# Kernel tuning notes

Hardware: AMD Instinct MI355X
Metric: run time of the kernel (lower is better)

## Reference

```python
import jax, jax.numpy as jnp
import numpy as np

B, T, N = 8, 168, 1024
FD, FS, FF = 16, 32, 8
DL, DG, HE, E = 128, 128, 4, 16384
BN = B * N


def _lstm_last(x, Wih, Whh, bih, bhh):
    # x: (BN, T, FD); PyTorch gate order i, f, g, o
    h0 = jnp.zeros((x.shape[0], Whh.shape[1]), x.dtype)
    def step(carry, xt):
        h, c = carry
        g = xt @ Wih.T + h @ Whh.T + bih + bhh
        i, f, gg, o = jnp.split(g, 4, axis=-1)
        c = jax.nn.sigmoid(f) * c + jax.nn.sigmoid(i) * jnp.tanh(gg)
        h = jax.nn.sigmoid(o) * jnp.tanh(c)
        return (h, c), None
    (h, _), _ = jax.lax.scan(step, (h0, h0), jnp.swapaxes(x, 0, 1))
    return h


def _ln(x, g, b):
    mu = x.mean(-1, keepdims=True)
    v = ((x - mu) ** 2).mean(-1, keepdims=True)
    return (x - mu) / jnp.sqrt(v + 1e-5) * g + b


def _gat(x, src, dst, ea, W, a_src, a_dst, a_edge, We, bias):
    # PyG GATConv: concat=False (mean over heads), edge_dim=1, LeakyReLU(0.2)
    xl = (x @ W.T).reshape(BN, HE, -1)                 # (BN, H, C)
    as_ = jnp.sum(xl * a_src, -1)                      # (BN, H)
    ad_ = jnp.sum(xl * a_dst, -1)
    ep = (ea @ We.T).reshape(-1, HE, xl.shape[-1])     # (Eb, H, C)
    ae_ = jnp.sum(ep * a_edge, -1)                     # (Eb, H)
    alpha = jax.nn.leaky_relu(as_[src] + ad_[dst] + ae_, 0.2)
    amax = jax.ops.segment_max(alpha, dst, num_segments=BN)
    ex = jnp.exp(alpha - amax[dst])
    den = jax.ops.segment_sum(ex, dst, num_segments=BN)
    w = ex / den[dst]                                  # softmax over incoming edges
    out = jax.ops.segment_sum(w[:, :, None] * xl[src], dst, num_segments=BN)
    return out.mean(axis=1) + bias


def _forward(fl, edge_index):
    (dyn, fcst, sta, ew,
     lWih, lWhh, lbih, lbhh, sW, sb, fW, fb, uW, ub,
     g0W, g0as, g0ad, g0ae, g0We, g0b,
     g1W, g1as, g1ad, g1ae, g1We, g1b,
     n0g, n0b, n1g, n1b, oW, ob) = fl
    x = jnp.transpose(dyn, (0, 2, 1, 3)).reshape(BN, T, FD)
    z = _lstm_last(x, lWih, lWhh, lbih, lbhh)
    s = jax.nn.relu(sta.reshape(BN, -1) @ sW.T + sb)
    f = jax.nn.relu(fcst.reshape(BN, -1) @ fW.T + fb)
    h = jax.nn.relu(jnp.concatenate([z, s, f], -1) @ uW.T + ub)
    # batch the graph: B disjoint copies with node offsets
    off = (jnp.arange(B) * N)[:, None]
    src = (edge_index[0][None] + off).reshape(-1)
    dst = (edge_index[1][None] + off).reshape(-1)
    ea = jnp.tile(ew.reshape(-1, 1), (B, 1))           # (B*E, 1)
    # PyG GATConv default add_self_loops=True, fill_value='mean' of incoming edge attrs
    deg = jax.ops.segment_sum(jnp.ones_like(ea), dst, num_segments=BN)
    loop_ea = jax.ops.segment_sum(ea, dst, num_segments=BN) / jnp.maximum(deg, 1.0)
    loops = jnp.arange(BN)
    src = jnp.concatenate([src, loops])
    dst = jnp.concatenate([dst, loops])
    ea = jnp.concatenate([ea, loop_ea], 0)
    # hop 0: relu on delta (not last hop), residual (res_proj=None since DL==DG), LayerNorm
    d0 = jax.nn.relu(_gat(h, src, dst, ea, g0W, g0as, g0ad, g0ae, g0We, g0b))
    h = _ln(h + d0, n0g, n0b)
    # hop 1: last hop, no relu on delta
    d1 = _gat(h, src, dst, ea, g1W, g1as, g1ad, g1ae, g1We, g1b)
    h = _ln(h + d1, n1g, n1b)
    return (h @ oW.T + ob).reshape(B, N)


def setup_inputs():
    key = jax.random.key(0)
    ks = iter(jax.random.split(key, 48))
    def rn(shape, s=0.08):
        return jax.random.normal(next(ks), shape, jnp.float32) * s
    HO = HE * DG  # heads * out_channels
    return dict(
        dynamic_features=rn((B, T, N, FD), 1.0),
        forecast_features=rn((B, N, FF), 1.0),
        static_features=rn((B, N, FS), 1.0),
        edge_index=jax.random.randint(next(ks), (2, E), 0, N),
        edge_weight=jax.random.uniform(next(ks), (E,), jnp.float32),
        lstm_Wih=rn((4 * DL, FD)), lstm_Whh=rn((4 * DL, DL)),
        lstm_bih=rn((4 * DL,)), lstm_bhh=rn((4 * DL,)),
        static_W=rn((DL, FS)), static_b=rn((DL,)),
        fcst_W=rn((DL, FF)), fcst_b=rn((DL,)),
        fusion_W=rn((DL, 3 * DL)), fusion_b=rn((DL,)),
        gat0_W=rn((HO, DL)), gat0_att_src=rn((1, HE, DG)), gat0_att_dst=rn((1, HE, DG)),
        gat0_att_edge=rn((1, HE, DG)), gat0_We=rn((HO, 1)), gat0_bias=rn((DG,)),
        gat1_W=rn((HO, DG)), gat1_att_src=rn((1, HE, DG)), gat1_att_dst=rn((1, HE, DG)),
        gat1_att_edge=rn((1, HE, DG)), gat1_We=rn((HO, 1)), gat1_bias=rn((DG,)),
        ln0_g=jnp.ones((DG,), jnp.float32), ln0_b=jnp.zeros((DG,), jnp.float32),
        ln1_g=jnp.ones((DG,), jnp.float32), ln1_b=jnp.zeros((DG,), jnp.float32),
        out_W=rn((1, DG)), out_b=rn((1,)),
    )


def reference(dynamic_features, forecast_features, static_features, edge_weight,
              lstm_Wih, lstm_Whh, lstm_bih, lstm_bhh, static_W, static_b,
              fcst_W, fcst_b, fusion_W, fusion_b,
              gat0_W, gat0_att_src, gat0_att_dst, gat0_att_edge, gat0_We, gat0_bias,
              gat1_W, gat1_att_src, gat1_att_dst, gat1_att_edge, gat1_We, gat1_bias,
              ln0_g, ln0_b, ln1_g, ln1_b, out_W, out_b, edge_index):
    fl = (dynamic_features, forecast_features, static_features, edge_weight,
          lstm_Wih, lstm_Whh, lstm_bih, lstm_bhh, static_W, static_b,
          fcst_W, fcst_b, fusion_W, fusion_b,
          gat0_W, gat0_att_src, gat0_att_dst, gat0_att_edge, gat0_We, gat0_bias,
          gat1_W, gat1_att_src, gat1_att_dst, gat1_att_edge, gat1_We, gat1_bias,
          ln0_g, ln0_b, ln1_g, ln1_b, out_W, out_b)
    return _forward(fl, edge_index)
```

## Files before the change

### kernel.cpp

```cpp
#include <hip/hip_runtime.h>
#include <hip/hip_bf16.h>
#include <stdint.h>

#define BB 8
#define TT 168
#define NN 1024
#define BN_ 8192
#define FD_ 16
#define EE 16384

typedef short short8 __attribute__((ext_vector_type(8)));
typedef __bf16 bf16x8 __attribute__((ext_vector_type(8)));
typedef float f32x4 __attribute__((ext_vector_type(4)));

#if __has_builtin(__builtin_amdgcn_exp2f)
#define EXP2(x) __builtin_amdgcn_exp2f(x)
#else
#define EXP2(x) exp2f(x)
#endif
#if __has_builtin(__builtin_amdgcn_rcpf)
#define RCPF(x) __builtin_amdgcn_rcpf(x)
#else
#define RCPF(x) (1.f / (x))
#endif
#define L2E 1.4426950408889634f
#define T2E 2.8853900817779268f

static __device__ __forceinline__ float b2f(ushort s) {
    unsigned u = ((unsigned)s) << 16;
    return __builtin_bit_cast(float, u);
}
static __device__ __forceinline__ ushort f2b(float f) {
    unsigned u = __builtin_bit_cast(unsigned, f);
    unsigned lsb = (u >> 16) & 1u;
    u += 0x7fffu + lsb;
    return (ushort)(u >> 16);
}
static __device__ __forceinline__ ushort f2b_fast(float f) {
    unsigned u = __builtin_bit_cast(unsigned, f);
    return (ushort)((u + 0x8000u) >> 16);
}
static __device__ __forceinline__ f32x4 mfma16(short8 a, short8 b, f32x4 c) {
    return __builtin_amdgcn_mfma_f32_16x16x32_bf16(
        __builtin_bit_cast(bf16x8, a), __builtin_bit_cast(bf16x8, b), c, 0, 0, 0);
}

#define O_WIH 0
#define O_WHH 8192
#define O_STA 73728
#define O_FCS 335872
#define O_SW  401408
#define O_FW  405504
#define O_UW  406528
#define O_G0W 455680
#define O_G1W 521216
#define O_END 586752

__global__ void cast_kernel(const float* __restrict__ Wih, const float* __restrict__ Whh,
                            const float* __restrict__ sta, const float* __restrict__ fcst,
                            const float* __restrict__ sW, const float* __restrict__ fW,
                            const float* __restrict__ uW, const float* __restrict__ g0W,
                            const float* __restrict__ g1W, ushort* __restrict__ dst) {
    const int i = blockIdx.x * 256 + threadIdx.x;
    if (i >= O_END) return;
    float v;
    if      (i < O_WHH) v = Wih[i - O_WIH];
    else if (i < O_STA) v = Whh[i - O_WHH];
    else if (i < O_FCS) v = sta[i - O_STA];
    else if (i < O_SW)  v = fcst[i - O_FCS];
    else if (i < O_FW)  v = sW[i - O_SW];
    else if (i < O_UW)  v = fW[i - O_FW];
    else if (i < O_G0W) v = uW[i - O_UW];
    else if (i < O_G1W) v = g0W[i - O_G0W];
    else                v = g1W[i - O_G1W];
    dst[i] = f2b(v);
}

__global__ __launch_bounds__(1024) void prep_kernel(
    const int* __restrict__ ei, const float* __restrict__ ew,
    const float* __restrict__ We0, const float* __restrict__ ae0,
    const float* __restrict__ We1, const float* __restrict__ ae1,
    int* __restrict__ deg0, int* __restrict__ offs, float* __restrict__ loopea,
    int* __restrict__ eidx, float* __restrict__ se) {
    __shared__ int degL[1024];
    __shared__ float wsL[1024];
    __shared__ int sc[1024];
    __shared__ float seL[8];
    const int t = threadIdx.x;
    degL[t] = 0; wsL[t] = 0.f;
    if (t < 8) seL[t] = 0.f;
    __syncthreads();
    for (int e = t; e < EE; e += 1024) {
        const int d = ei[EE + e];
        atomicAdd(&degL[d], 1);
        atomicAdd(&wsL[d], ew[e]);
    }
    __syncthreads();
    const int d = degL[t];
    sc[t] = d;
    __syncthreads();
    for (int o = 1; o < 1024; o <<= 1) {
        const int v = (t >= o) ? sc[t - o] : 0;
        __syncthreads();
        sc[t] += v;
        __syncthreads();
    }
    const int excl = sc[t] - d;
    offs[t] = excl;
    deg0[t] = d;
    loopea[t] = wsL[t] / fmaxf((float)d, 1.f);
    degL[t] = excl;
    __syncthreads();
    for (int e = t; e < EE; e += 1024) {
        const int dd = ei[EE + e];
        const int slot = atomicAdd(&degL[dd], 1);
        eidx[slot] = e;
    }
    const int g = t >> 7, k = t & 127;
    const int head = g & 3;
    const float* W = (g >> 2) ? We1 : We0;
    const float* A = (g >> 2) ? ae1 : ae0;
    atomicAdd(&seL[g], W[head * 128 + k] * A[head * 128 + k]);
    __syncthreads();
    if (t < 8) se[t] = seL[t];
}

__global__ __launch_bounds__(256, 2) void lstm_kernel(
    const float* __restrict__ dyn,
    const ushort* __restrict__ Wih,
    const ushort* __restrict__ Whh,
    const float* __restrict__ bih,
    const float* __restrict__ bhh,
    ushort* __restrict__ zsf)
{
    constexpr int HS = 168;
    __shared__ ushort hbuf[2][16 * HS];

    const int tid = threadIdx.x;
    const int blk = blockIdx.x;
    const int b = blk >> 6;
    const int n0 = (blk & 63) << 4;
    const int w = tid >> 6, lane = tid & 63, quad = lane >> 4, m = lane & 15;

    short8 Bf[5][4][2];
    float ci[2], cf[2], cg[2], co[2];
#pragma unroll
    for (int jj = 0; jj < 2; jj++) {
        const int u = (2 * w + jj) * 16 + m;
#pragma unroll
        for (int g = 0; g < 4; g++) {
            const int grow = g * 128 + u;
#pragma unroll
            for (int kt = 0; kt < 4; kt++)
                Bf[kt][g][jj] = *(const short8*)(Whh + grow * 128 + kt * 32 + quad * 8);
            if (quad < 2) Bf[4][g][jj] = *(const short8*)(Wih + grow * 16 + quad * 8);
            else          Bf[4][g][jj] = short8{0, 0, 0, 0, 0, 0, 0, 0};
        }
        ci[jj] = -L2E * (bih[u] + bhh[u]);
        cf[jj] = -L2E * (bih[128 + u] + bhh[128 + u]);
        cg[jj] =  T2E * (bih[256 + u] + bhh[256 + u]);
        co[jj] = -L2E * (bih[384 + u] + bhh[384 + u]);
    }

    float c[2][4];
#pragma unroll
    for (int jj = 0; jj < 2; jj++)
#pragma unroll
        for (int r = 0; r < 4; r++) c[jj][r] = 0.f;

    for (int i = tid; i < 2 * 16 * HS; i += 256) ((ushort*)hbuf)[i] = 0;
    __syncthreads();

    const int xn = tid >> 4, xf = tid & 15;
    const size_t xbase = (size_t)b * TT * NN * FD_ + (size_t)(n0 + xn) * FD_ + xf;
    hbuf[0][xn * HS + 128 + xf] = f2b(dyn[xbase]);
    float xv = dyn[xbase + (size_t)NN * FD_];
    __syncthreads();

    for (int t = 0; t < TT; t++) {
        const ushort* rb = hbuf[t & 1];
        ushort* wb = hbuf[(t + 1) & 1];
        if (t + 1 < TT) wb[xn * HS + 128 + xf] = f2b(xv);
        if (t + 2 < TT) xv = dyn[xbase + (size_t)(t + 2) * NN * FD_];

        f32x4 acc[4][2];
#pragma unroll
        for (int g = 0; g < 4; g++)
#pragma unroll
            for (int jj = 0; jj < 2; jj++) acc[g][jj] = f32x4{0.f, 0.f, 0.f, 0.f};
#pragma unroll
        for (int kt = 0; kt < 5; kt++) {
            short8 a = *(const short8*)&rb[m * HS + kt * 32 + quad * 8];
#pragma unroll
            for (int g = 0; g < 4; g++)
#pragma unroll
                for (int jj = 0; jj < 2; jj++)
                    acc[g][jj] = mfma16(a, Bf[kt][g][jj], acc[g][jj]);
        }

#pragma unroll
        for (int jj = 0; jj < 2; jj++) {
            const int u = (2 * w + jj) * 16 + m;
#pragma unroll
            for (int r = 0; r < 4; r++) {
                const int n = quad * 4 + r;
                const float Di = 1.f + EXP2(fmaf(acc[0][jj][r], -L2E, ci[jj]));
                const float Df = 1.f + EXP2(fmaf(acc[1][jj][r], -L2E, cf[jj]));
                const float Eg = EXP2(fmaf(acc[2][jj][r], T2E, cg[jj]));
                const float Do = 1.f + EXP2(fmaf(acc[3][jj][r], -L2E, co[jj]));
                const float R  = RCPF(Di * (1.f + Eg));
                const float sf = RCPF(Df);
                const float cc = fmaf(sf, c[jj][r], (Eg - 1.f) * R);
                c[jj][r] = cc;
                const float Ec = EXP2(T2E * cc);
                const float h = (Ec - 1.f) * RCPF(Do * (1.f + Ec));
                wb[n * HS + u] = f2b_fast(h);
                if (t == TT - 1) zsf[(size_t)(blk * 16 + n) * 384 + u] = f2b_fast(h);
            }
        }
        __syncthreads();
    }
}

__global__ __launch_bounds__(256) void gemm_sf_kernel(
    const ushort* __restrict__ staB, const ushort* __restrict__ sWB,
    const float* __restrict__ sb,
    const ushort* __restrict__ fcsB, const ushort* __restrict__ fWB,
    const float* __restrict__ fb, ushort* __restrict__ zsf) {
    const int tid = threadIdx.x;
    const int lane = tid & 63, quad = lane >> 4, m = lane & 15;
    int wave = blockIdx.x * 4 + (tid >> 6);
    const short8 z8 = short8{0, 0, 0, 0, 0, 0, 0, 0};
    short8 a, bf;
    int r0, c0, ocol;
    const float* bias;
    if (wave < 4096) {
        r0 = (wave >> 3) * 16; c0 = (wave & 7) * 16; ocol = 128; bias = sb;
        a  = *(const short8*)(staB + (size_t)(r0 + m) * 32 + quad * 8);
        bf = *(const short8*)(sWB + (size_t)(c0 + m) * 32 + quad * 8);
    } else {
        wave -= 4096;
        r0 = (wave >> 3) * 16; c0 = (wave & 7) * 16; ocol = 256; bias = fb;
        a  = (quad == 0) ? *(const short8*)(fcsB + (size_t)(r0 + m) * 8) : z8;
        bf = (quad == 0) ? *(const short8*)(fWB + (size_t)(c0 + m) * 8) : z8;
    }
    f32x4 acc = mfma16(a, bf, f32x4{0.f, 0.f, 0.f, 0.f});
    const float bv = bias[c0 + m];
#pragma unroll
    for (int r = 0; r < 4; r++) {
        const int row = r0 + quad * 4 + r;
        zsf[(size_t)row * 384 + ocol + c0 + m] = f2b(fmaxf(acc[r] + bv, 0.f));
    }
}

__global__ __launch_bounds__(256) void gemm_fusion_kernel(
    const ushort* __restrict__ A, const ushort* __restrict__ Bt,
    const float* __restrict__ bias, ushort* __restrict__ hB, float* __restrict__ hF) {
    const int tid = threadIdx.x;
    const int lane = tid & 63, quad = lane >> 4, m = lane & 15;
    const int wave = blockIdx.x * 4 + (tid >> 6);
    const int r0 = (wave >> 3) * 16, c0 = (wave & 7) * 16;
    f32x4 acc = f32x4{0.f, 0.f, 0.f, 0.f};
#pragma unroll
    for (int kt = 0; kt < 12; kt++) {
        const int k = kt * 32 + quad * 8;
        short8 a  = *(const short8*)(A + (size_t)(r0 + m) * 384 + k);
        short8 bf = *(const short8*)(Bt + (size_t)(c0 + m) * 384 + k);
        acc = mfma16(a, bf, acc);
    }
    const int col = c0 + m;
    const float bv = bias[col];
#pragma unroll
    for (int r = 0; r < 4; r++) {
        const int row = r0 + quad * 4 + r;
        const float v = fmaxf(acc[r] + bv, 0.f);
        hB[(size_t)row * 128 + col] = f2b(v);
        hF[(size_t)row * 128 + col] = v;
    }
}

__global__ __launch_bounds__(256) void gemmatt_kernel(
    const ushort* __restrict__ hB, const ushort* __restrict__ W,
    const float* __restrict__ asrc, const float* __restrict__ adst,
    ushort* __restrict__ xl, float* __restrict__ as_, float* __restrict__ ad_) {
    const int tid = threadIdx.x;
    const int lane = tid & 63, quad = lane >> 4, m = lane & 15;
    const int w = tid >> 6;
    const int r0 = blockIdx.x * 16;
    f32x4 acc[8];
#pragma unroll
    for (int ct = 0; ct < 8; ct++) acc[ct] = f32x4{0.f, 0.f, 0.f, 0.f};
#pragma unroll
    for (int kt = 0; kt < 4; kt++) {
        const int k = kt * 32 + quad * 8;
        short8 a = *(const short8*)(hB + (size_t)(r0 + m) * 128 + k);
#pragma unroll
        for (int ct = 0; ct < 8; ct++) {
            short8 bf = *(const short8*)(W + (size_t)(w * 128 + ct * 16 + m) * 128 + k);
            acc[ct] = mfma16(a, bf, acc[ct]);
        }
    }
    float sa[4] = {0.f, 0.f, 0.f, 0.f}, sd[4] = {0.f, 0.f, 0.f, 0.f};
#pragma unroll
    for (int ct = 0; ct < 8; ct++) {
        const int col = w * 128 + ct * 16 + m;
        const float av = asrc[col], dv = adst[col];
#pragma unroll
        for (int r = 0; r < 4; r++) {
            const float v = acc[ct][r];
            xl[(size_t)(r0 + quad * 4 + r) * 512 + col] = f2b(v);
            sa[r] = fmaf(v, av, sa[r]);
            sd[r] = fmaf(v, dv, sd[r]);
        }
    }
#pragma unroll
    for (int o = 1; o < 16; o <<= 1) {
#pragma unroll
        for (int r = 0; r < 4; r++) {
            sa[r] += __shfl_xor(sa[r], o);
            sd[r] += __shfl_xor(sd[r], o);
        }
    }
    if (m == 0) {
#pragma unroll
        for (int r = 0; r < 4; r++) {
            const int node = r0 + quad * 4 + r;
            as_[node * 4 + w] = sa[r];
            ad_[node * 4 + w] = sd[r];
        }
    }
}

__global__ __launch_bounds__(256) void edge_exp_kernel(
    const int* __restrict__ ei, const float* __restrict__ ew,
    const float* __restrict__ as_, const float* __restrict__ ad_,
    const float* __restrict__ se4, float* __restrict__ pexp) {
    const int idx = blockIdx.x * 256 + threadIdx.x;
    const int b = idx >> 14, e = idx & (EE - 1);
    const int src = b * 1024 + ei[e];
    const int dst = b * 1024 + ei[EE + e];
    const float eaw = ew[e];
    const float4 s4 = *(const float4*)(as_ + src * 4);
    const float4 d4 = *(const float4*)(ad_ + dst * 4);
    float4 p;
    float* pp = (float*)&p;
    const float* s = (const float*)&s4;
    const float* d = (const float*)&d4;
#pragma unroll
    for (int h = 0; h < 4; h++) {
        float a = s[h] + d[h] + eaw * se4[h];
        a = (a < 0.f) ? 0.2f * a : a;
        pp[h] = EXP2(fminf(a, 60.f) * L2E);
    }
    *(float4*)(pexp + (size_t)idx * 4) = p;
}

__global__ __launch_bounds__(256) void gat_kernel(
    float* __restrict__ hF, ushort* __restrict__ hB, const ushort* __restrict__ xl,
    const float* __restrict__ as_, const float* __restrict__ ad_,
    const float* __restrict__ pexp,
    const int* __restrict__ eidx, const int* __restrict__ offs,
    const int* __restrict__ deg0, const float* __restrict__ loopea,
    const int* __restrict__ ei,
    const float* __restrict__ se4, const float* __restrict__ bias,
    const float* __restrict__ lng, const float* __restrict__ lnb, int relu,
    int writeOut, const float* __restrict__ oW, const float* __restrict__ ob,
    float* __restrict__ out) {
    const int lane = threadIdx.x & 63;
    const int v = blockIdx.x * 4 + (threadIdx.x >> 6);
    const int b = v >> 10, n = v & 1023;
    const int dg = deg0[n], off = offs[n];

    const float lea = loopea[n];
    const float4 s4 = *(const float4*)(as_ + v * 4);
    const float4 d4 = *(const float4*)(ad_ + v * 4);
    const float* sp = (const float*)&s4;
    const float* dp = (const float*)&d4;
    float den[4], num0[4], num1[4];
#pragma unroll
    for (int h = 0; h < 4; h++) {
        float a = sp[h] + dp[h] + lea * se4[h];
        a = (a < 0.f) ? 0.2f * a : a;
        const float p = EXP2(fminf(a, 60.f) * L2E);
        den[h] = p;
        num0[h] = p * b2f(xl[(size_t)v * 512 + h * 128 + lane]);
        num1[h] = p * b2f(xl[(size_t)v * 512 + h * 128 + 64 + lane]);
    }
    for (int i = 0; i < dg; i++) {
        const int e = eidx[off + i];
        const int src = b * 1024 + ei[e];
        const float4 p4 = *(const float4*)(pexp + (size_t)(b * EE + e) * 4);
        const float* p = (const float*)&p4;
        const ushort* xr = xl + (size_t)src * 512;
#pragma unroll
        for (int h = 0; h < 4; h++) {
            den[h] += p[h];
            num0[h] = fmaf(p[h], b2f(xr[h * 128 + lane]), num0[h]);
            num1[h] = fmaf(p[h], b2f(xr[h * 128 + 64 + lane]), num1[h]);
        }
    }
    float o0 = 0.f, o1 = 0.f;
#pragma unroll
    for (int h = 0; h < 4; h++) {
        const float inv = RCPF(den[h]);
        o0 = fmaf(num0[h], inv, o0);
        o1 = fmaf(num1[h], inv, o1);
    }

    float d0 = o0 * 0.25f + bias[lane];
    float d1 = o1 * 0.25f + bias[64 + lane];
    if (relu) { d0 = fmaxf(d0, 0.f); d1 = fmaxf(d1, 0.f); }
    const float x0 = hF[(size_t)v * 128 + lane] + d0;
    const float x1 = hF[(size_t)v * 128 + 64 + lane] + d1;

    float s = x0 + x1;
#pragma unroll
    for (int o = 32; o; o >>= 1) s += __shfl_xor(s, o);
    const float mu = s * (1.f / 128.f);
    const float e0 = x0 - mu, e1 = x1 - mu;
    float vs = e0 * e0 + e1 * e1;
#pragma unroll
    for (int o = 32; o; o >>= 1) vs += __shfl_xor(vs, o);
    const float r = rsqrtf(vs * (1.f / 128.f) + 1e-5f);
    const float y0 = e0 * r * lng[lane] + lnb[lane];
    const float y1 = e1 * r * lng[64 + lane] + lnb[64 + lane];
    if (writeOut) {
        float t = y0 * oW[lane] + y1 * oW[64 + lane];
#pragma unroll
        for (int o = 32; o; o >>= 1) t += __shfl_xor(t, o);
        if (lane == 0) out[v] = t + ob[0];
    } else {
        hF[(size_t)v * 128 + lane] = y0;
        hF[(size_t)v * 128 + 64 + lane] = y1;
        hB[(size_t)v * 128 + lane] = f2b(y0);
        hB[(size_t)v * 128 + 64 + lane] = f2b(y1);
    }
}

extern "C" void kernel_launch(void* const* d_in, const int* in_sizes, int n_in,
                              void* d_out, int out_size, void* d_ws, size_t ws_size,
                              hipStream_t stream) {
    const float* dyn  = (const float*)d_in[0];
    const float* fcst = (const float*)d_in[1];
    const float* sta  = (const float*)d_in[2];
    const int*   ei   = (const int*)d_in[3];
    const float* ew   = (const float*)d_in[4];
    const float* lWih = (const float*)d_in[5];
    const float* lWhh = (const float*)d_in[6];
    const float* lbih = (const float*)d_in[7];
    const float* lbhh = (const float*)d_in[8];
    const float* sW = (const float*)d_in[9];
    const float* sb = (const float*)d_in[10];
    const float* fW = (const float*)d_in[11];
    const float* fb = (const float*)d_in[12];
    const float* uW = (const float*)d_in[13];
    const float* ub = (const float*)d_in[14];
    const float* g0W  = (const float*)d_in[15];
    const float* g0as = (const float*)d_in[16];
    const float* g0ad = (const float*)d_in[17];
    const float* g0ae = (const float*)d_in[18];
    const float* g0We = (const float*)d_in[19];
    const float* g0b  = (const float*)d_in[20];
    const float* g1W  = (const float*)d_in[21];
    const float* g1as = (const float*)d_in[22];
    const float* g1ad = (const float*)d_in[23];
    const float* g1ae = (const float*)d_in[24];
    const float* g1We = (const float*)d_in[25];
    const float* g1b  = (const float*)d_in[26];
    const float* ln0g = (const float*)d_in[27];
    const float* ln0b = (const float*)d_in[28];
    const float* ln1g = (const float*)d_in[29];
    const float* ln1b = (const float*)d_in[30];
    const float* oW = (const float*)d_in[31];
    const float* ob = (const float*)d_in[32];

    char* p = (char*)d_ws;
    ushort* castB = (ushort*)p; p += (size_t)O_END * 2 + 512;
    ushort* zsf = (ushort*)p;  p += (size_t)BN_ * 384 * 2;
    float*  hF  = (float*)p;   p += (size_t)BN_ * 128 * 4;
    ushort* hB  = (ushort*)p;  p += (size_t)BN_ * 128 * 2;
    ushort* xl  = (ushort*)p;  p += (size_t)BN_ * 512 * 2;
    float*  asb = (float*)p;   p += (size_t)BN_ * 4 * 4;
    float*  adb = (float*)p;   p += (size_t)BN_ * 4 * 4;
    int*    deg0   = (int*)p;   p += 4096;
    int*    offs   = (int*)p;   p += 4096;
    float*  loopea = (float*)p; p += 4096;
    int*    eidx   = (int*)p;   p += (size_t)EE * 4;
    float*  se     = (float*)p; p += 256;
    float*  pexp   = (float*)zsf;

    const ushort* WihB = castB + O_WIH;
    const ushort* WhhB = castB + O_WHH;
    const ushort* staB = castB + O_STA;
    const ushort* fcsB = castB + O_FCS;
    const ushort* sWB  = castB + O_SW;
    const ushort* fWB  = castB + O_FW;
    const ushort* uWB  = castB + O_UW;
    const ushort* g0WB = castB + O_G0W;
    const ushort* g1WB = castB + O_G1W;

    cast_kernel<<<(O_END + 255) / 256, 256, 0, stream>>>(lWih, lWhh, sta, fcst, sW, fW,
                                                         uW, g0W, g1W, castB);
    prep_kernel<<<1, 1024, 0, stream>>>(ei, ew, g0We, g0ae, g1We, g1ae,
                                        deg0, offs, loopea, eidx, se);

    lstm_kernel<<<512, 256, 0, stream>>>(dyn, WihB, WhhB, lbih, lbhh, zsf);
    gemm_sf_kernel<<<2048, 256, 0, stream>>>(staB, sWB, sb, fcsB, fWB, fb, zsf);
    gemm_fusion_kernel<<<1024, 256, 0, stream>>>(zsf, uWB, ub, hB, hF);

    gemmatt_kernel<<<512, 256, 0, stream>>>(hB, g0WB, g0as, g0ad, xl, asb, adb);
    edge_exp_kernel<<<512, 256, 0, stream>>>(ei, ew, asb, adb, se, pexp);
    gat_kernel<<<2048, 256, 0, stream>>>(hF, hB, xl, asb, adb, pexp, eidx, offs, deg0,
                                         loopea, ei, se, g0b, ln0g, ln0b, 1,
                                         0, oW, ob, (float*)d_out);
    gemmatt_kernel<<<512, 256, 0, stream>>>(hB, g1WB, g1as, g1ad, xl, asb, adb);
    edge_exp_kernel<<<512, 256, 0, stream>>>(ei, ew, asb, adb, se + 4, pexp);
    gat_kernel<<<2048, 256, 0, stream>>>(hF, hB, xl, asb, adb, pexp, eidx, offs, deg0,
                                         loopea, ei, se + 4, g1b, ln1g, ln1b, 0,
                                         1, oW, ob, (float*)d_out);
}
```

Before: 580.2 us.

## Widen LSTM blocks, fold graph prep into sf GEMM, fuse edge softmax into GAT

The LSTM kernel now runs 512 threads per block, with each wave owning 16 hidden units instead of 32. This halves per-thread register state and is meant to raise occupancy and MFMA parallelism. The single-block prep kernel is merged as an extra block into the static/forecast GEMM launch, removing a serial launch. The edge_exp kernel is removed and attention logits are recomputed inside the GAT aggregation loop, which drops the pexp buffer traffic at the cost of redundant exp and source-attention loads per edge.

```diff
diff --git a/kernel.cpp b/kernel.cpp
--- a/kernel.cpp
+++ b/kernel.cpp
@@ -76,56 +76,7 @@
     dst[i] = f2b(v);
 }
 
-__global__ __launch_bounds__(1024) void prep_kernel(
-    const int* __restrict__ ei, const float* __restrict__ ew,
-    const float* __restrict__ We0, const float* __restrict__ ae0,
-    const float* __restrict__ We1, const float* __restrict__ ae1,
-    int* __restrict__ deg0, int* __restrict__ offs, float* __restrict__ loopea,
-    int* __restrict__ eidx, float* __restrict__ se) {
-    __shared__ int degL[1024];
-    __shared__ float wsL[1024];
-    __shared__ int sc[1024];
-    __shared__ float seL[8];
-    const int t = threadIdx.x;
-    degL[t] = 0; wsL[t] = 0.f;
-    if (t < 8) seL[t] = 0.f;
-    __syncthreads();
-    for (int e = t; e < EE; e += 1024) {
-        const int d = ei[EE + e];
-        atomicAdd(&degL[d], 1);
-        atomicAdd(&wsL[d], ew[e]);
-    }
-    __syncthreads();
-    const int d = degL[t];
-    sc[t] = d;
-    __syncthreads();
-    for (int o = 1; o < 1024; o <<= 1) {
-        const int v = (t >= o) ? sc[t - o] : 0;
-        __syncthreads();
-        sc[t] += v;
-        __syncthreads();
-    }
-    const int excl = sc[t] - d;
-    offs[t] = excl;
-    deg0[t] = d;
-    loopea[t] = wsL[t] / fmaxf((float)d, 1.f);
-    degL[t] = excl;
-    __syncthreads();
-    for (int e = t; e < EE; e += 1024) {
-        const int dd = ei[EE + e];
-        const int slot = atomicAdd(&degL[dd], 1);
-        eidx[slot] = e;
-    }
-    const int g = t >> 7, k = t & 127;
-    const int head = g & 3;
-    const float* W = (g >> 2) ? We1 : We0;
-    const float* A = (g >> 2) ? ae1 : ae0;
-    atomicAdd(&seL[g], W[head * 128 + k] * A[head * 128 + k]);
-    __syncthreads();
-    if (t < 8) se[t] = seL[t];
-}
-
-__global__ __launch_bounds__(256, 2) void lstm_kernel(
+__global__ __launch_bounds__(512, 4) void lstm_kernel(
     const float* __restrict__ dyn,
     const ushort* __restrict__ Wih,
     const ushort* __restrict__ Whh,
@@ -141,116 +92,168 @@
     const int b = blk >> 6;
     const int n0 = (blk & 63) << 4;
     const int w = tid >> 6, lane = tid & 63, quad = lane >> 4, m = lane & 15;
-
-    short8 Bf[5][4][2];
-    float ci[2], cf[2], cg[2], co[2];
-#pragma unroll
-    for (int jj = 0; jj < 2; jj++) {
-        const int u = (2 * w + jj) * 16 + m;
-#pragma unroll
-        for (int g = 0; g < 4; g++) {
-            const int grow = g * 128 + u;
-#pragma unroll
-            for (int kt = 0; kt < 4; kt++)
-                Bf[kt][g][jj] = *(const short8*)(Whh + grow * 128 + kt * 32 + quad * 8);
-            if (quad < 2) Bf[4][g][jj] = *(const short8*)(Wih + grow * 16 + quad * 8);
-            else          Bf[4][g][jj] = short8{0, 0, 0, 0, 0, 0, 0, 0};
-        }
-        ci[jj] = -L2E * (bih[u] + bhh[u]);
-        cf[jj] = -L2E * (bih[128 + u] + bhh[128 + u]);
-        cg[jj] =  T2E * (bih[256 + u] + bhh[256 + u]);
-        co[jj] = -L2E * (bih[384 + u] + bhh[384 + u]);
-    }
-
-    float c[2][4];
-#pragma unroll
-    for (int jj = 0; jj < 2; jj++)
-#pragma unroll
-        for (int r = 0; r < 4; r++) c[jj][r] = 0.f;
-
-    for (int i = tid; i < 2 * 16 * HS; i += 256) ((ushort*)hbuf)[i] = 0;
+    const int u = w * 16 + m;
+
+    short8 Bf[5][4];
+    float ci, cf, cg, co;
+#pragma unroll
+    for (int g = 0; g < 4; g++) {
+        const int grow = g * 128 + u;
+#pragma unroll
+        for (int kt = 0; kt < 4; kt++)
+            Bf[kt][g] = *(const short8*)(Whh + grow * 128 + kt * 32 + quad * 8);
+        if (quad < 2) Bf[4][g] = *(const short8*)(Wih + grow * 16 + quad * 8);
+        else          Bf[4][g] = short8{0, 0, 0, 0, 0, 0, 0, 0};
+    }
+    ci = -L2E * (bih[u] + bhh[u]);
+    cf = -L2E * (bih[128 + u] + bhh[128 + u]);
+    cg =  T2E * (bih[256 + u] + bhh[256 + u]);
+    co = -L2E * (bih[384 + u] + bhh[384 + u]);
+
+    float c[4];
+#pragma unroll
+    for (int r = 0; r < 4; r++) c[r] = 0.f;
+
+    for (int i = tid; i < 2 * 16 * HS; i += 512) ((ushort*)hbuf)[i] = 0;
     __syncthreads();
 
     const int xn = tid >> 4, xf = tid & 15;
     const size_t xbase = (size_t)b * TT * NN * FD_ + (size_t)(n0 + xn) * FD_ + xf;
-    hbuf[0][xn * HS + 128 + xf] = f2b(dyn[xbase]);
-    float xv = dyn[xbase + (size_t)NN * FD_];
+    float xv = 0.f;
+    if (tid < 256) {
+        hbuf[0][xn * HS + 128 + xf] = f2b(dyn[xbase]);
+        xv = dyn[xbase + (size_t)NN * FD_];
+    }
     __syncthreads();
 
     for (int t = 0; t < TT; t++) {
         const ushort* rb = hbuf[t & 1];
         ushort* wb = hbuf[(t + 1) & 1];
-        if (t + 1 < TT) wb[xn * HS + 128 + xf] = f2b(xv);
-        if (t + 2 < TT) xv = dyn[xbase + (size_t)(t + 2) * NN * FD_];
-
-        f32x4 acc[4][2];
-#pragma unroll
-        for (int g = 0; g < 4; g++)
-#pragma unroll
-            for (int jj = 0; jj < 2; jj++) acc[g][jj] = f32x4{0.f, 0.f, 0.f, 0.f};
+        if (tid < 256) {
+            if (t + 1 < TT) wb[xn * HS + 128 + xf] = f2b(xv);
+            if (t + 2 < TT) xv = dyn[xbase + (size_t)(t + 2) * NN * FD_];
+        }
+
+        f32x4 acc[4];
+#pragma unroll
+        for (int g = 0; g < 4; g++) acc[g] = f32x4{0.f, 0.f, 0.f, 0.f};
 #pragma unroll
         for (int kt = 0; kt < 5; kt++) {
             short8 a = *(const short8*)&rb[m * HS + kt * 32 + quad * 8];
 #pragma unroll
             for (int g = 0; g < 4; g++)
-#pragma unroll
-                for (int jj = 0; jj < 2; jj++)
-                    acc[g][jj] = mfma16(a, Bf[kt][g][jj], acc[g][jj]);
-        }
-
-#pragma unroll
-        for (int jj = 0; jj < 2; jj++) {
-            const int u = (2 * w + jj) * 16 + m;
-#pragma unroll
-            for (int r = 0; r < 4; r++) {
-                const int n = quad * 4 + r;
-                const float Di = 1.f + EXP2(fmaf(acc[0][jj][r], -L2E, ci[jj]));
-                const float Df = 1.f + EXP2(fmaf(acc[1][jj][r], -L2E, cf[jj]));
-                const float Eg = EXP2(fmaf(acc[2][jj][r], T2E, cg[jj]));
-                const float Do = 1.f + EXP2(fmaf(acc[3][jj][r], -L2E, co[jj]));
-                const float R  = RCPF(Di * (1.f + Eg));
-                const float sf = RCPF(Df);
-                const float cc = fmaf(sf, c[jj][r], (Eg - 1.f) * R);
-                c[jj][r] = cc;
-                const float Ec = EXP2(T2E * cc);
-                const float h = (Ec - 1.f) * RCPF(Do * (1.f + Ec));
-                wb[n * HS + u] = f2b_fast(h);
-                if (t == TT - 1) zsf[(size_t)(blk * 16 + n) * 384 + u] = f2b_fast(h);
-            }
+                acc[g] = mfma16(a, Bf[kt][g], acc[g]);
+        }
+
+#pragma unroll
+        for (int r = 0; r < 4; r++) {
+            const int n = quad * 4 + r;
+            const float Di = 1.f + EXP2(fmaf(acc[0][r], -L2E, ci));
+            const float Df = 1.f + EXP2(fmaf(acc[1][r], -L2E, cf));
+            const float Eg = EXP2(fmaf(acc[2][r], T2E, cg));
+            const float Do = 1.f + EXP2(fmaf(acc[3][r], -L2E, co));
+            const float R  = RCPF(Di * (1.f + Eg));
+            const float sf = RCPF(Df);
+            const float cc = fmaf(sf, c[r], (Eg - 1.f) * R);
+            c[r] = cc;
+            const float Ec = EXP2(T2E * cc);
+            const float h = (Ec - 1.f) * RCPF(Do * (1.f + Ec));
+            wb[n * HS + u] = f2b_fast(h);
+            if (t == TT - 1) zsf[(size_t)(blk * 16 + n) * 384 + u] = f2b_fast(h);
         }
         __syncthreads();
     }
 }
 
-__global__ __launch_bounds__(256) void gemm_sf_kernel(
+__global__ __launch_bounds__(256) void gemm_sf_prep_kernel(
     const ushort* __restrict__ staB, const ushort* __restrict__ sWB,
     const float* __restrict__ sb,
     const ushort* __restrict__ fcsB, const ushort* __restrict__ fWB,
-    const float* __restrict__ fb, ushort* __restrict__ zsf) {
+    const float* __restrict__ fb, ushort* __restrict__ zsf,
+    const int* __restrict__ ei, const float* __restrict__ ew,
+    const float* __restrict__ We0, const float* __restrict__ ae0,
+    const float* __restrict__ We1, const float* __restrict__ ae1,
+    int* __restrict__ deg0, int* __restrict__ offs, float* __restrict__ loopea,
+    int* __restrict__ eidx, float* __restrict__ se) {
     const int tid = threadIdx.x;
-    const int lane = tid & 63, quad = lane >> 4, m = lane & 15;
-    int wave = blockIdx.x * 4 + (tid >> 6);
-    const short8 z8 = short8{0, 0, 0, 0, 0, 0, 0, 0};
-    short8 a, bf;
-    int r0, c0, ocol;
-    const float* bias;
-    if (wave < 4096) {
-        r0 = (wave >> 3) * 16; c0 = (wave & 7) * 16; ocol = 128; bias = sb;
-        a  = *(const short8*)(staB + (size_t)(r0 + m) * 32 + quad * 8);
-        bf = *(const short8*)(sWB + (size_t)(c0 + m) * 32 + quad * 8);
-    } else {
-        wave -= 4096;
-        r0 = (wave >> 3) * 16; c0 = (wave & 7) * 16; ocol = 256; bias = fb;
-        a  = (quad == 0) ? *(const short8*)(fcsB + (size_t)(r0 + m) * 8) : z8;
-        bf = (quad == 0) ? *(const short8*)(fWB + (size_t)(c0 + m) * 8) : z8;
-    }
-    f32x4 acc = mfma16(a, bf, f32x4{0.f, 0.f, 0.f, 0.f});
-    const float bv = bias[c0 + m];
-#pragma unroll
-    for (int r = 0; r < 4; r++) {
-        const int row = r0 + quad * 4 + r;
-        zsf[(size_t)row * 384 + ocol + c0 + m] = f2b(fmaxf(acc[r] + bv, 0.f));
-    }
+    if (blockIdx.x < 2048) {
+        const int lane = tid & 63, quad = lane >> 4, m = lane & 15;
+        int wave = blockIdx.x * 4 + (tid >> 6);
+        const short8 z8 = short8{0, 0, 0, 0, 0, 0, 0, 0};
+        short8 a, bf;
+        int r0, c0, ocol;
+        const float* bias;
+        if (wave < 4096) {
+            r0 = (wave >> 3) * 16; c0 = (wave & 7) * 16; ocol = 128; bias = sb;
+            a  = *(const short8*)(staB + (size_t)(r0 + m) * 32 + quad * 8);
+            bf = *(const short8*)(sWB + (size_t)(c0 + m) * 32 + quad * 8);
+        } else {
+            wave -= 4096;
+            r0 = (wave >> 3) * 16; c0 = (wave & 7) * 16; ocol = 256; bias = fb;
+            a  = (quad == 0) ? *(const short8*)(fcsB + (size_t)(r0 + m) * 8) : z8;
+            bf = (quad == 0) ? *(const short8*)(fWB + (size_t)(c0 + m) * 8) : z8;
+        }
+        f32x4 acc = mfma16(a, bf, f32x4{0.f, 0.f, 0.f, 0.f});
+        const float bv = bias[c0 + m];
+#pragma unroll
+        for (int r = 0; r < 4; r++) {
+            const int row = r0 + quad * 4 + r;
+            zsf[(size_t)row * 384 + ocol + c0 + m] = f2b(fmaxf(acc[r] + bv, 0.f));
+        }
+        return;
+    }
+    __shared__ int degL[1024];
+    __shared__ float wsL[1024];
+    __shared__ int part[256];
+    __shared__ float seL[8];
+    for (int i = tid; i < 1024; i += 256) { degL[i] = 0; wsL[i] = 0.f; }
+    if (tid < 8) seL[tid] = 0.f;
+    __syncthreads();
+    for (int e = tid; e < EE; e += 256) {
+        const int d = ei[EE + e];
+        atomicAdd(&degL[d], 1);
+        atomicAdd(&wsL[d], ew[e]);
+    }
+    __syncthreads();
+    const int d0 = degL[4 * tid], d1 = degL[4 * tid + 1];
+    const int d2 = degL[4 * tid + 2], d3 = degL[4 * tid + 3];
+    const int tot = d0 + d1 + d2 + d3;
+    part[tid] = tot;
+    __syncthreads();
+    for (int o = 1; o < 256; o <<= 1) {
+        const int v = (tid >= o) ? part[tid - o] : 0;
+        __syncthreads();
+        part[tid] += v;
+        __syncthreads();
+    }
+    int base = part[tid] - tot;
+    int ex[4];
+    ex[0] = base; ex[1] = base + d0; ex[2] = ex[1] + d1; ex[3] = ex[2] + d2;
+    const int dd4[4] = {d0, d1, d2, d3};
+#pragma unroll
+    for (int j = 0; j < 4; j++) {
+        const int n = 4 * tid + j;
+        offs[n] = ex[j];
+        deg0[n] = dd4[j];
+        loopea[n] = wsL[n] / fmaxf((float)dd4[j], 1.f);
+    }
+    __syncthreads();
+#pragma unroll
+    for (int j = 0; j < 4; j++) degL[4 * tid + j] = ex[j];
+    __syncthreads();
+    for (int e = tid; e < EE; e += 256) {
+        const int dd = ei[EE + e];
+        const int slot = atomicAdd(&degL[dd], 1);
+        eidx[slot] = e;
+    }
+    for (int i = tid; i < 1024; i += 256) {
+        const int g = i >> 7, k = i & 127, head = g & 3;
+        const float* W = (g >> 2) ? We1 : We0;
+        const float* A = (g >> 2) ? ae1 : ae0;
+        atomicAdd(&seL[g], W[head * 128 + k] * A[head * 128 + k]);
+    }
+    __syncthreads();
+    if (tid < 8) se[tid] = seL[tid];
 }
 
 __global__ __launch_bounds__(256) void gemm_fusion_kernel(
@@ -331,37 +334,12 @@
     }
 }
 
-__global__ __launch_bounds__(256) void edge_exp_kernel(
-    const int* __restrict__ ei, const float* __restrict__ ew,
-    const float* __restrict__ as_, const float* __restrict__ ad_,
-    const float* __restrict__ se4, float* __restrict__ pexp) {
-    const int idx = blockIdx.x * 256 + threadIdx.x;
-    const int b = idx >> 14, e = idx & (EE - 1);
-    const int src = b * 1024 + ei[e];
-    const int dst = b * 1024 + ei[EE + e];
-    const float eaw = ew[e];
-    const float4 s4 = *(const float4*)(as_ + src * 4);
-    const float4 d4 = *(const float4*)(ad_ + dst * 4);
-    float4 p;
-    float* pp = (float*)&p;
-    const float* s = (const float*)&s4;
-    const float* d = (const float*)&d4;
-#pragma unroll
-    for (int h = 0; h < 4; h++) {
-        float a = s[h] + d[h] + eaw * se4[h];
-        a = (a < 0.f) ? 0.2f * a : a;
-        pp[h] = EXP2(fminf(a, 60.f) * L2E);
-    }
-    *(float4*)(pexp + (size_t)idx * 4) = p;
-}
-
 __global__ __launch_bounds__(256) void gat_kernel(
     float* __restrict__ hF, ushort* __restrict__ hB, const ushort* __restrict__ xl,
     const float* __restrict__ as_, const float* __restrict__ ad_,
-    const float* __restrict__ pexp,
     const int* __restrict__ eidx, const int* __restrict__ offs,
     const int* __restrict__ deg0, const float* __restrict__ loopea,
-    const int* __restrict__ ei,
+    const int* __restrict__ ei, const float* __restrict__ ew,
     const float* __restrict__ se4, const float* __restrict__ bias,
     const float* __restrict__ lng, const float* __restrict__ lnb, int relu,
     int writeOut, const float* __restrict__ oW, const float* __restrict__ ob,
@@ -371,6 +349,10 @@
     const int b = v >> 10, n = v & 1023;
     const int dg = deg0[n], off = offs[n];
 
+    float se[4];
+#pragma unroll
+    for (int h = 0; h < 4; h++) se[h] = se4[h];
+
     const float lea = loopea[n];
     const float4 s4 = *(const float4*)(as_ + v * 4);
     const float4 d4 = *(const float4*)(ad_ + v * 4);
@@ -379,7 +361,7 @@
     float den[4], num0[4], num1[4];
 #pragma unroll
     for (int h = 0; h < 4; h++) {
-        float a = sp[h] + dp[h] + lea * se4[h];
+        float a = sp[h] + dp[h] + lea * se[h];
         a = (a < 0.f) ? 0.2f * a : a;
         const float p = EXP2(fminf(a, 60.f) * L2E);
         den[h] = p;
@@ -389,14 +371,18 @@
     for (int i = 0; i < dg; i++) {
         const int e = eidx[off + i];
         const int src = b * 1024 + ei[e];
-        const float4 p4 = *(const float4*)(pexp + (size_t)(b * EE + e) * 4);
-        const float* p = (const float*)&p4;
+        const float eaw = ew[e];
+        const float4 ss4 = *(const float4*)(as_ + src * 4);
+        const float* ssp = (const float*)&ss4;
         const ushort* xr = xl + (size_t)src * 512;
 #pragma unroll
         for (int h = 0; h < 4; h++) {
-            den[h] += p[h];
-            num0[h] = fmaf(p[h], b2f(xr[h * 128 + lane]), num0[h]);
-            num1[h] = fmaf(p[h], b2f(xr[h * 128 + 64 + lane]), num1[h]);
+            float a = ssp[h] + dp[h] + eaw * se[h];
+            a = (a < 0.f) ? 0.2f * a : a;
+            const float p = EXP2(fminf(a, 60.f) * L2E);
+            den[h] += p;
+            num0[h] = fmaf(p, b2f(xr[h * 128 + lane]), num0[h]);
+            num1[h] = fmaf(p, b2f(xr[h * 128 + 64 + lane]), num1[h]);
         }
     }
     float o0 = 0.f, o1 = 0.f;
@@ -487,7 +473,6 @@
     float*  loopea = (float*)p; p += 4096;
     int*    eidx   = (int*)p;   p += (size_t)EE * 4;
     float*  se     = (float*)p; p += 256;
-    float*  pexp   = (float*)zsf;
 
     const ushort* WihB = castB + O_WIH;
     const ushort* WhhB = castB + O_WHH;
@@ -501,21 +486,18 @@
 
     cast_kernel<<<(O_END + 255) / 256, 256, 0, stream>>>(lWih, lWhh, sta, fcst, sW, fW,
                                                          uW, g0W, g1W, castB);
-    prep_kernel<<<1, 1024, 0, stream>>>(ei, ew, g0We, g0ae, g1We, g1ae,
-                                        deg0, offs, loopea, eidx, se);
-
-    lstm_kernel<<<512, 256, 0, stream>>>(dyn, WihB, WhhB, lbih, lbhh, zsf);
-    gemm_sf_kernel<<<2048, 256, 0, stream>>>(staB, sWB, sb, fcsB, fWB, fb, zsf);
+    lstm_kernel<<<512, 512, 0, stream>>>(dyn, WihB, WhhB, lbih, lbhh, zsf);
+    gemm_sf_prep_kernel<<<2049, 256, 0, stream>>>(staB, sWB, sb, fcsB, fWB, fb, zsf,
+                                                  ei, ew, g0We, g0ae, g1We, g1ae,
+                                                  deg0, offs, loopea, eidx, se);
     gemm_fusion_kernel<<<1024, 256, 0, stream>>>(zsf, uWB, ub, hB, hF);
 
     gemmatt_kernel<<<512, 256, 0, stream>>>(hB, g0WB, g0as, g0ad, xl, asb, adb);
-    edge_exp_kernel<<<512, 256, 0, stream>>>(ei, ew, asb, adb, se, pexp);
-    gat_kernel<<<2048, 256, 0, stream>>>(hF, hB, xl, asb, adb, pexp, eidx, offs, deg0,
-                                         loopea, ei, se, g0b, ln0g, ln0b, 1,
+    gat_kernel<<<2048, 256, 0, stream>>>(hF, hB, xl, asb, adb, eidx, offs, deg0,
+                                         loopea, ei, ew, se, g0b, ln0g, ln0b, 1,
                                          0, oW, ob, (float*)d_out);
     gemmatt_kernel<<<512, 256, 0, stream>>>(hB, g1WB, g1as, g1ad, xl, asb, adb);
-    edge_exp_kernel<<<512, 256, 0, stream>>>(ei, ew, asb, adb, se + 4, pexp);
-    gat_kernel<<<2048, 256, 0, stream>>>(hF, hB, xl, asb, adb, pexp, eidx, offs, deg0,
-                                         loopea, ei, se + 4, g1b, ln1g, ln1b, 0,
+    gat_kernel<<<2048, 256, 0, stream>>>(hF, hB, xl, asb, adb, eidx, offs, deg0,
+                                         loopea, ei, ew, se + 4, g1b, ln1g, ln1b, 0,
                                          1, oW, ob, (float*)d_out);
 }
```

After: 605.1 us. 1.04x slower.
